# Kernel optimization log

Measured on AMD Instinct MI355X. Metric: run time of the kernel, lower is better.

## Reference

```python
import jax, jax.numpy as jnp
import numpy as np

N_NODES = 200000
FEAT_DIM = 256
EMB_DIM = 64
N_EXP = 100000
N_TARGETS = 1024
MAX_CAND = 128


def setup_inputs() -> dict:
    key = jax.random.key(0)
    ks = jax.random.split(key, 10)
    return {
        "x": jax.random.normal(ks[0], (N_NODES, FEAT_DIM), jnp.float32),
        "h": jax.random.normal(ks[1], (N_NODES, EMB_DIM), jnp.float32),
        "degree": jax.random.uniform(ks[2], (N_NODES,), jnp.float32),
        "beta": jax.random.uniform(ks[3], (N_NODES,), jnp.float32),
        "exp_nodes": jax.random.randint(ks[4], (N_EXP,), 0, N_NODES),
        "idx_targets": jax.random.randint(ks[5], (N_TARGETS,), 0, N_NODES),
        "W_raw": jax.random.normal(ks[6], (FEAT_DIM, EMB_DIM), jnp.float32) / np.float32(np.sqrt(FEAT_DIM)),
        "b_raw": jnp.zeros((EMB_DIM,), jnp.float32),
        "W_num": jax.random.normal(ks[7], (2, EMB_DIM), jnp.float32),
        "b_num": jnp.zeros((EMB_DIM,), jnp.float32),
        "W1": jax.random.normal(ks[8], (4 * EMB_DIM, EMB_DIM), jnp.float32) / np.float32(np.sqrt(4 * EMB_DIM)),
        "b1": jnp.zeros((EMB_DIM,), jnp.float32),
        "W2": jax.random.normal(ks[9], (EMB_DIM, 1), jnp.float32) / np.float32(np.sqrt(EMB_DIM)),
        "b2": jnp.zeros((1,), jnp.float32),
        "temperature": jnp.float32(1.0),
        "epsilon": jnp.float32(1.0),
    }


def reference(x, h, degree, beta, exp_nodes, idx_targets,
              W_raw, b_raw, W_num, b_num, W1, b1, W2, b2,
              temperature, epsilon):
    # gather node features and project (irregular gather + small GEMM)
    x_v = x[exp_nodes] @ W_raw + b_raw                       # [E, emb]
    h_v = h[exp_nodes]                                       # [E, emb]
    h_T = jnp.broadcast_to(h[idx_targets].mean(axis=0)[None, :],
                           (exp_nodes.shape[0], EMB_DIM))    # [E, emb]
    numerics = jnp.stack([degree[exp_nodes], beta[exp_nodes]], axis=-1)  # [E, 2]
    emb_num = numerics @ W_num + b_num                       # [E, emb]
    emb = jax.nn.relu(jnp.concatenate([x_v, h_v, h_T, emb_num], axis=-1))  # [E, 4*emb]
    # dropout is identity in eval mode
    hidden = jax.nn.relu(emb @ W1 + b1)                      # [E, emb]
    scores = (hidden @ W2 + b2)[:, 0]                        # [E]
    # straight-through gumbel top-k (eval: no gumbel noise, epsilon unused)
    y = jax.nn.softmax(scores / temperature)
    _, idx = jax.lax.top_k(y, MAX_CAND)
    y_hard = jnp.zeros_like(y).at[idx].set(1.0)
    y_st = jax.lax.stop_gradient(y_hard - y) + y
    candidates = y_st[idx]                                   # [MAX_CAND] (== 1.0 fwd)
    cand_indices = exp_nodes[idx]                            # [MAX_CAND]
    return candidates, cand_indices
```

## Files before the change

### kernel.cpp

```cpp
#include <hip/hip_runtime.h>
#include <stdint.h>

#define RELU(v) ((v) > 0.0f ? (v) : 0.0f)

typedef unsigned long long u64;
typedef unsigned int u32;
typedef unsigned short u16;
typedef float f32x4 __attribute__((ext_vector_type(4)));
typedef short bf16x8 __attribute__((ext_vector_type(8)));

constexpr int FEAT = 256;
constexpr int EMB  = 64;

constexpr int STG_ROW = 264;
constexpr int WAVE_BYTES = 16 * STG_ROW * 2;
constexpr int XV_ROW = 68;
constexpr int KEEP_BLK = 12;

__device__ inline u16 bf16_trunc(float v) { return (u16)(__float_as_uint(v) >> 16); }

__device__ inline u32 score_key(float s) {
    u32 u = __float_as_uint(s);
    return (u & 0x80000000u) ? ~u : (u | 0x80000000u);
}

__device__ inline bf16x8 pack_bf16x8(float4 lo, float4 hi) {
    bf16x8 r;
    r[0] = (short)bf16_trunc(lo.x); r[1] = (short)bf16_trunc(lo.y);
    r[2] = (short)bf16_trunc(lo.z); r[3] = (short)bf16_trunc(lo.w);
    r[4] = (short)bf16_trunc(hi.x); r[5] = (short)bf16_trunc(hi.y);
    r[6] = (short)bf16_trunc(hi.z); r[7] = (short)bf16_trunc(hi.w);
    return r;
}

__global__ __launch_bounds__(1024) void setup_kernel(
    const float* __restrict__ h, const int* __restrict__ idx_targets, int nT,
    const float* __restrict__ W_raw, const float* __restrict__ W1, const float* __restrict__ b1,
    float* __restrict__ bias_eff, u16* __restrict__ wrawpk, u16* __restrict__ w1pk)
{
    const int tid = threadIdx.x;
    if (blockIdx.x == 1) {
        for (int t = tid; t < 2048; t += 1024) {
            int ks   = t >> 8;
            int c    = (t >> 6) & 3;
            int lane = t & 63;
            int n    = c * 16 + (lane & 15);
            int kbase = ks * 32 + ((lane >> 4) << 3);
            #pragma unroll
            for (int j = 0; j < 8; ++j) {
                int k = kbase + j;
                wrawpk[t * 8 + j] = bf16_trunc(W_raw[(size_t)k * EMB + n]);
                w1pk  [t * 8 + j] = bf16_trunc(W1   [(size_t)k * EMB + n]);
            }
        }
        return;
    }
    __shared__ int   idx_s[1024];
    __shared__ float partial[16][64];
    __shared__ float hT[64];
    const int nid = nT > 1024 ? 1024 : nT;
    for (int i = tid; i < nid; i += 1024) idx_s[i] = idx_targets[i];
    __syncthreads();
    const int d = tid & 63, grp = tid >> 6;
    float s = 0.f;
    for (int t = grp; t < nid; t += 16)
        s += h[(size_t)idx_s[t] * EMB + d];
    partial[grp][d] = s;
    __syncthreads();
    if (tid < 64) {
        float m = 0.f;
        #pragma unroll
        for (int g = 0; g < 16; ++g) m += partial[g][tid];
        hT[tid] = RELU(m / (float)nT);
    }
    __syncthreads();
    if (tid < 64) {
        float acc = b1[tid];
        #pragma unroll 8
        for (int dd = 0; dd < 64; ++dd)
            acc = fmaf(hT[dd], W1[(size_t)(128 + dd) * EMB + tid], acc);
        bias_eff[tid] = acc;
    }
}

__global__ __launch_bounds__(256) void approx_score_kernel(
    const float* __restrict__ x, const float* __restrict__ h,
    const float* __restrict__ degree, const float* __restrict__ beta,
    const int* __restrict__ exp_nodes,
    const u16* __restrict__ wrawpk, const u16* __restrict__ w1pk,
    const float* __restrict__ b_raw,
    const float* __restrict__ W_num, const float* __restrict__ b_num,
    const float* __restrict__ W2, const float* __restrict__ bias_eff,
    u64* __restrict__ cand1, int E)
{
    __shared__ __align__(16) unsigned char smem[4][WAVE_BYTES];
    __shared__ u64 sarr[64];

    const int tid  = threadIdx.x;
    const int wid  = tid >> 6;
    const int lane = tid & 63;
    const int rloc = lane & 15;
    const int kgrp = lane >> 4;
    const int koff = kgrp * 8;
    const int tileBase = blockIdx.x * 64;

    const int grow = tileBase + wid * 16 + rloc;
    const int node = exp_nodes[grow < E ? grow : 0];
    const float* hrow = h + (size_t)node * EMB;
    const float dg = degree[node];
    const float bt = beta[node];

    u16*   stg = (u16*)&smem[wid][0];
    float* xvp = (float*)&smem[wid][0];

    {
        float4 v0  = *reinterpret_cast<const float4*>(x + (size_t)__shfl(node,  0) * FEAT + lane * 4);
        float4 v1  = *reinterpret_cast<const float4*>(x + (size_t)__shfl(node,  1) * FEAT + lane * 4);
        float4 v2  = *reinterpret_cast<const float4*>(x + (size_t)__shfl(node,  2) * FEAT + lane * 4);
        float4 v3  = *reinterpret_cast<const float4*>(x + (size_t)__shfl(node,  3) * FEAT + lane * 4);
        float4 v4  = *reinterpret_cast<const float4*>(x + (size_t)__shfl(node,  4) * FEAT + lane * 4);
        float4 v5  = *reinterpret_cast<const float4*>(x + (size_t)__shfl(node,  5) * FEAT + lane * 4);
        float4 v6  = *reinterpret_cast<const float4*>(x + (size_t)__shfl(node,  6) * FEAT + lane * 4);
        float4 v7  = *reinterpret_cast<const float4*>(x + (size_t)__shfl(node,  7) * FEAT + lane * 4);
        float4 v8  = *reinterpret_cast<const float4*>(x + (size_t)__shfl(node,  8) * FEAT + lane * 4);
        float4 v9  = *reinterpret_cast<const float4*>(x + (size_t)__shfl(node,  9) * FEAT + lane * 4);
        float4 v10 = *reinterpret_cast<const float4*>(x + (size_t)__shfl(node, 10) * FEAT + lane * 4);
        float4 v11 = *reinterpret_cast<const float4*>(x + (size_t)__shfl(node, 11) * FEAT + lane * 4);
        float4 v12 = *reinterpret_cast<const float4*>(x + (size_t)__shfl(node, 12) * FEAT + lane * 4);
        float4 v13 = *reinterpret_cast<const float4*>(x + (size_t)__shfl(node, 13) * FEAT + lane * 4);
        float4 v14 = *reinterpret_cast<const float4*>(x + (size_t)__shfl(node, 14) * FEAT + lane * 4);
        float4 v15 = *reinterpret_cast<const float4*>(x + (size_t)__shfl(node, 15) * FEAT + lane * 4);
        #define STG_WRITE(rr, vv) { \
            ushort4 pk; pk.x = bf16_trunc(vv.x); pk.y = bf16_trunc(vv.y); \
            pk.z = bf16_trunc(vv.z); pk.w = bf16_trunc(vv.w); \
            *reinterpret_cast<ushort4*>(stg + (rr) * STG_ROW + lane * 4) = pk; }
        STG_WRITE( 0, v0)  STG_WRITE( 1, v1)  STG_WRITE( 2, v2)  STG_WRITE( 3, v3)
        STG_WRITE( 4, v4)  STG_WRITE( 5, v5)  STG_WRITE( 6, v6)  STG_WRITE( 7, v7)
        STG_WRITE( 8, v8)  STG_WRITE( 9, v9)  STG_WRITE(10, v10) STG_WRITE(11, v11)
        STG_WRITE(12, v12) STG_WRITE(13, v13) STG_WRITE(14, v14) STG_WRITE(15, v15)
        #undef STG_WRITE
    }
    __builtin_amdgcn_wave_barrier();

    f32x4 acc1[4];
    #pragma unroll
    for (int c = 0; c < 4; ++c) {
        float bv = b_raw[c * 16 + rloc];
        acc1[c] = (f32x4){bv, bv, bv, bv};
    }
    #pragma unroll
    for (int ks = 0; ks < 8; ++ks) {
        bf16x8 a = *reinterpret_cast<const bf16x8*>(stg + rloc * STG_ROW + ks * 32 + koff);
        #pragma unroll
        for (int c = 0; c < 4; ++c) {
            bf16x8 b = *reinterpret_cast<const bf16x8*>(wrawpk + (size_t)((ks * 4 + c) * 64 + lane) * 8);
            acc1[c] = __builtin_amdgcn_mfma_f32_16x16x32_bf16(a, b, acc1[c], 0, 0, 0);
        }
    }
    __builtin_amdgcn_wave_barrier();

    #pragma unroll
    for (int c = 0; c < 4; ++c)
        #pragma unroll
        for (int r = 0; r < 4; ++r)
            xvp[(kgrp * 4 + r) * XV_ROW + c * 16 + rloc] = RELU(acc1[c][r]);
    __builtin_amdgcn_wave_barrier();

    f32x4 acc2[4];
    #pragma unroll
    for (int c = 0; c < 4; ++c) {
        float bv = bias_eff[c * 16 + rloc];
        acc2[c] = (f32x4){bv, bv, bv, bv};
    }

    #pragma unroll
    for (int ks = 0; ks < 2; ++ks) {
        float4 lo = *reinterpret_cast<const float4*>(hrow + ks * 32 + koff);
        float4 hi = *reinterpret_cast<const float4*>(hrow + ks * 32 + koff + 4);
        lo.x = RELU(lo.x); lo.y = RELU(lo.y); lo.z = RELU(lo.z); lo.w = RELU(lo.w);
        hi.x = RELU(hi.x); hi.y = RELU(hi.y); hi.z = RELU(hi.z); hi.w = RELU(hi.w);
        bf16x8 a = pack_bf16x8(lo, hi);
        #pragma unroll
        for (int c = 0; c < 4; ++c) {
            bf16x8 b = *reinterpret_cast<const bf16x8*>(w1pk + (size_t)(((2 + ks) * 4 + c) * 64 + lane) * 8);
            acc2[c] = __builtin_amdgcn_mfma_f32_16x16x32_bf16(a, b, acc2[c], 0, 0, 0);
        }
    }

    #pragma unroll
    for (int ks = 0; ks < 2; ++ks) {
        bf16x8 a;
        #pragma unroll
        for (int j = 0; j < 8; ++j) {
            int k = ks * 32 + koff + j;
            float v = RELU(fmaf(dg, W_num[k], fmaf(bt, W_num[EMB + k], b_num[k])));
            a[j] = (short)bf16_trunc(v);
        }
        #pragma unroll
        for (int c = 0; c < 4; ++c) {
            bf16x8 b = *reinterpret_cast<const bf16x8*>(w1pk + (size_t)(((6 + ks) * 4 + c) * 64 + lane) * 8);
            acc2[c] = __builtin_amdgcn_mfma_f32_16x16x32_bf16(a, b, acc2[c], 0, 0, 0);
        }
    }

    #pragma unroll
    for (int ks = 0; ks < 2; ++ks) {
        float4 lo = *reinterpret_cast<const float4*>(xvp + rloc * XV_ROW + ks * 32 + koff);
        float4 hi = *reinterpret_cast<const float4*>(xvp + rloc * XV_ROW + ks * 32 + koff + 4);
        bf16x8 a = pack_bf16x8(lo, hi);
        #pragma unroll
        for (int c = 0; c < 4; ++c) {
            bf16x8 b = *reinterpret_cast<const bf16x8*>(w1pk + (size_t)((ks * 4 + c) * 64 + lane) * 8);
            acc2[c] = __builtin_amdgcn_mfma_f32_16x16x32_bf16(a, b, acc2[c], 0, 0, 0);
        }
    }

    float p[4] = {0.f, 0.f, 0.f, 0.f};
    #pragma unroll
    for (int c = 0; c < 4; ++c) {
        float w2v = W2[c * 16 + rloc];
        #pragma unroll
        for (int r = 0; r < 4; ++r)
            p[r] = fmaf(RELU(acc2[c][r]), w2v, p[r]);
    }
    #pragma unroll
    for (int m = 1; m < 16; m <<= 1) {
        p[0] += __shfl_xor(p[0], m);
        p[1] += __shfl_xor(p[1], m);
        p[2] += __shfl_xor(p[2], m);
        p[3] += __shfl_xor(p[3], m);
    }
    if (rloc == 0) {
        #pragma unroll
        for (int r = 0; r < 4; ++r) {
            int lrow = wid * 16 + kgrp * 4 + r;
            int g = tileBase + lrow;
            sarr[lrow] = (g < E) ? (((u64)score_key(p[r]) << 32) | (u32)(~(u32)g)) : 0ULL;
        }
    }
    __syncthreads();

    if (wid == 0) {
        u64 v = sarr[lane];
        #pragma unroll
        for (int k = 2; k <= 64; k <<= 1) {
            #pragma unroll
            for (int j = k >> 1; j > 0; j >>= 1) {
                u64 o = __shfl_xor(v, j);
                bool lower = (lane & j) == 0;
                bool dir   = (lane & k) == 0;
                v = (lower == dir) ? (v > o ? v : o) : (v < o ? v : o);
            }
        }
        if (lane < KEEP_BLK) cand1[(size_t)blockIdx.x * KEEP_BLK + lane] = v;
    }
}

template<int N, int NT>
__device__ inline void bitonic_desc(u64* s, int tid) {
    for (int k = 2; k <= N; k <<= 1) {
        for (int j = k >> 1; j > 0; j >>= 1) {
            __syncthreads();
            for (int i = tid; i < N; i += NT) {
                int ixj = i ^ j;
                if (ixj > i) {
                    u64 a = s[i], b = s[ixj];
                    bool sw = ((i & k) == 0) ? (a < b) : (a > b);
                    if (sw) { s[i] = b; s[ixj] = a; }
                }
            }
        }
    }
    __syncthreads();
}

template<int N, int NT, int KEEP>
__global__ __launch_bounds__(NT) void seg_sort_kernel(
    const u64* __restrict__ in, int n_in, int seg, u64* __restrict__ out)
{
    __shared__ u64 s[N];
    int tid = threadIdx.x;
    int base = blockIdx.x * seg;
    for (int i = tid; i < N; i += NT) {
        int g = base + i;
        s[i] = (i < seg && g < n_in) ? in[g] : 0ULL;
    }
    bitonic_desc<N, NT>(s, tid);
    if (tid < KEEP) out[blockIdx.x * KEEP + tid] = s[tid];
}

__global__ __launch_bounds__(256) void rescore_kernel(
    const float* __restrict__ x, const float* __restrict__ h,
    const float* __restrict__ degree, const float* __restrict__ beta,
    const int* __restrict__ exp_nodes,
    const float* __restrict__ W_raw, const float* __restrict__ b_raw,
    const float* __restrict__ W_num, const float* __restrict__ b_num,
    const float* __restrict__ W1, const float* __restrict__ W2,
    const float* __restrict__ bias_eff,
    const u64* __restrict__ cand, u64* __restrict__ pairs2, int E)
{
    __shared__ float emb[4][192];
    const int tid = threadIdx.x;
    const int wid = tid >> 6;
    const int c   = tid & 63;
    const int i   = blockIdx.x * 4 + wid;

    const u64 raw = cand[i];
    const u32 low = (u32)raw;
    const u32 ge  = ~low;
    const int node = (raw != 0ULL && ge < (u32)E) ? exp_nodes[ge] : 0;

    const float* xrow = x + (size_t)node * FEAT;

    float s0 = b_raw[c], s1 = 0.f, s2 = 0.f, s3 = 0.f;
    for (int k = 0; k < FEAT; k += 4) {
        s0 = fmaf(xrow[k + 0], W_raw[(size_t)(k + 0) * EMB + c], s0);
        s1 = fmaf(xrow[k + 1], W_raw[(size_t)(k + 1) * EMB + c], s1);
        s2 = fmaf(xrow[k + 2], W_raw[(size_t)(k + 2) * EMB + c], s2);
        s3 = fmaf(xrow[k + 3], W_raw[(size_t)(k + 3) * EMB + c], s3);
    }
    float xv = (s0 + s1) + (s2 + s3);

    emb[wid][c]       = RELU(xv);
    emb[wid][64 + c]  = RELU(h[(size_t)node * EMB + c]);
    emb[wid][128 + c] = RELU(fmaf(degree[node], W_num[c], fmaf(beta[node], W_num[EMB + c], b_num[c])));
    __syncthreads();

    float h0 = bias_eff[c], h1 = 0.f, h2 = 0.f, h3 = 0.f;
    for (int j = 0; j < 64; j += 2) {
        h0 = fmaf(emb[wid][j],     W1[(size_t)j * EMB + c],       h0);
        h1 = fmaf(emb[wid][j + 1], W1[(size_t)(j + 1) * EMB + c], h1);
    }
    for (int j = 0; j < 64; j += 2) {
        h2 = fmaf(emb[wid][64 + j],     W1[(size_t)(64 + j) * EMB + c],     h2);
        h3 = fmaf(emb[wid][64 + j + 1], W1[(size_t)(64 + j + 1) * EMB + c], h3);
    }
    for (int j = 0; j < 64; j += 2) {
        h0 = fmaf(emb[wid][128 + j],     W1[(size_t)(192 + j) * EMB + c],     h0);
        h1 = fmaf(emb[wid][128 + j + 1], W1[(size_t)(192 + j + 1) * EMB + c], h1);
    }
    float hid = (h0 + h1) + (h2 + h3);

    float p = RELU(hid) * W2[c];
    #pragma unroll
    for (int m = 1; m < 64; m <<= 1) p += __shfl_xor(p, m);

    if (c == 0)
        pairs2[i] = (raw == 0ULL) ? 0ULL : (((u64)score_key(p) << 32) | low);
}

__global__ __launch_bounds__(1024) void topk_final_kernel(
    const u64* __restrict__ in, int n_in,
    const int* __restrict__ exp_nodes, float* __restrict__ out)
{
    __shared__ u64 s[1024];
    int tid = threadIdx.x;
    s[tid] = (tid < n_in) ? in[tid] : 0ULL;
    bitonic_desc<1024, 1024>(s, tid);
    if (tid < 128) {
        u64 p = s[tid];
        u32 idx = ~(u32)(p & 0xFFFFFFFFu);
        out[tid]       = 1.0f;
        out[128 + tid] = (float)exp_nodes[idx];
    }
}

extern "C" void kernel_launch(void* const* d_in, const int* in_sizes, int n_in,
                              void* d_out, int out_size, void* d_ws, size_t ws_size,
                              hipStream_t stream) {
    const float* x          = (const float*)d_in[0];
    const float* h          = (const float*)d_in[1];
    const float* degree     = (const float*)d_in[2];
    const float* beta       = (const float*)d_in[3];
    const int*   exp_nodes  = (const int*)d_in[4];
    const int*   idx_targets= (const int*)d_in[5];
    const float* W_raw      = (const float*)d_in[6];
    const float* b_raw      = (const float*)d_in[7];
    const float* W_num      = (const float*)d_in[8];
    const float* b_num      = (const float*)d_in[9];
    const float* W1         = (const float*)d_in[10];
    const float* b1         = (const float*)d_in[11];
    const float* W2         = (const float*)d_in[12];

    int E  = in_sizes[4];
    int nT = in_sizes[5];

    int nTiles = (E + 63) / 64;
    int nCand1 = nTiles * KEEP_BLK;
    int nSel   = (nCand1 + 1023) / 1024;
    int nKept  = nSel * 52;
    int nResc  = (nKept + 3) / 4;

    char* ws = (char*)d_ws;
    float* bias_eff = (float*)ws;
    u16* wrawpk = (u16*)(ws + 256);
    u16* w1pk   = (u16*)(ws + 256 + 32768);
    u64* cand1  = (u64*)(ws + 256 + 65536);
    u64* cand2  = (u64*)(ws + 256 + 65536 + 163840);
    u64* pairs2 = (u64*)(ws + 256 + 65536 + 163840 + 8192);

    setup_kernel<<<2, 1024, 0, stream>>>(h, idx_targets, nT, W_raw, W1, b1,
                                         bias_eff, wrawpk, w1pk);

    approx_score_kernel<<<nTiles, 256, 0, stream>>>(x, h, degree, beta, exp_nodes,
                                                    wrawpk, w1pk, b_raw, W_num, b_num,
                                                    W2, bias_eff, cand1, E);

    seg_sort_kernel<1024, 512, 52><<<nSel, 512, 0, stream>>>(cand1, nCand1, 1024, cand2);

    rescore_kernel<<<nResc, 256, 0, stream>>>(x, h, degree, beta, exp_nodes,
                                              W_raw, b_raw, W_num, b_num, W1, W2,
                                              bias_eff, cand2, pairs2, E);

    topk_final_kernel<<<1, 1024, 0, stream>>>(pairs2, nKept, exp_nodes, (float*)d_out);
}
```

Measured before the change: 106.8 us.

## Fuse segment sort and exact rescoring into one kernel with finer segments

Replaces the separate segment-sort and rescore kernels with one kernel. Each of 64 blocks loads a segment of about 300 approximate-score candidates into a 512-entry shared-memory bitonic sort, then rescores its top 16 exactly, using wave-level barriers instead of block barriers. This removes one kernel launch, the round trip through the intermediate candidate buffer, and uses a smaller sort per block. The trade-off is that only 16 candidates per segment survive instead of 52 per 1024, so a segment holding more than 16 of the true top 128 would now drop some.

```diff
diff --git a/kernel.cpp b/kernel.cpp
--- a/kernel.cpp
+++ b/kernel.cpp
@@ -274,22 +274,8 @@
     __syncthreads();
 }
 
-template<int N, int NT, int KEEP>
-__global__ __launch_bounds__(NT) void seg_sort_kernel(
-    const u64* __restrict__ in, int n_in, int seg, u64* __restrict__ out)
-{
-    __shared__ u64 s[N];
-    int tid = threadIdx.x;
-    int base = blockIdx.x * seg;
-    for (int i = tid; i < N; i += NT) {
-        int g = base + i;
-        s[i] = (i < seg && g < n_in) ? in[g] : 0ULL;
-    }
-    bitonic_desc<N, NT>(s, tid);
-    if (tid < KEEP) out[blockIdx.x * KEEP + tid] = s[tid];
-}
-
-__global__ __launch_bounds__(256) void rescore_kernel(
+__global__ __launch_bounds__(512) void selrescore_kernel(
+    const u64* __restrict__ cand1, int nCand1, int seg,
     const float* __restrict__ x, const float* __restrict__ h,
     const float* __restrict__ degree, const float* __restrict__ beta,
     const int* __restrict__ exp_nodes,
@@ -297,56 +283,69 @@
     const float* __restrict__ W_num, const float* __restrict__ b_num,
     const float* __restrict__ W1, const float* __restrict__ W2,
     const float* __restrict__ bias_eff,
-    const u64* __restrict__ cand, u64* __restrict__ pairs2, int E)
+    u64* __restrict__ pairs2, int E)
 {
-    __shared__ float emb[4][192];
+    __shared__ u64  s[512];
+    __shared__ float emb[8][192];
     const int tid = threadIdx.x;
+    const int base = blockIdx.x * seg;
+
+    for (int i = tid; i < 512; i += 512) {
+        int g = base + i;
+        s[i] = (i < seg && g < nCand1) ? cand1[g] : 0ULL;
+    }
+    bitonic_desc<512, 512>(s, tid);
+
     const int wid = tid >> 6;
     const int c   = tid & 63;
-    const int i   = blockIdx.x * 4 + wid;
-
-    const u64 raw = cand[i];
-    const u32 low = (u32)raw;
-    const u32 ge  = ~low;
-    const int node = (raw != 0ULL && ge < (u32)E) ? exp_nodes[ge] : 0;
-
-    const float* xrow = x + (size_t)node * FEAT;
-
-    float s0 = b_raw[c], s1 = 0.f, s2 = 0.f, s3 = 0.f;
-    for (int k = 0; k < FEAT; k += 4) {
-        s0 = fmaf(xrow[k + 0], W_raw[(size_t)(k + 0) * EMB + c], s0);
-        s1 = fmaf(xrow[k + 1], W_raw[(size_t)(k + 1) * EMB + c], s1);
-        s2 = fmaf(xrow[k + 2], W_raw[(size_t)(k + 2) * EMB + c], s2);
-        s3 = fmaf(xrow[k + 3], W_raw[(size_t)(k + 3) * EMB + c], s3);
-    }
-    float xv = (s0 + s1) + (s2 + s3);
-
-    emb[wid][c]       = RELU(xv);
-    emb[wid][64 + c]  = RELU(h[(size_t)node * EMB + c]);
-    emb[wid][128 + c] = RELU(fmaf(degree[node], W_num[c], fmaf(beta[node], W_num[EMB + c], b_num[c])));
-    __syncthreads();
-
-    float h0 = bias_eff[c], h1 = 0.f, h2 = 0.f, h3 = 0.f;
-    for (int j = 0; j < 64; j += 2) {
-        h0 = fmaf(emb[wid][j],     W1[(size_t)j * EMB + c],       h0);
-        h1 = fmaf(emb[wid][j + 1], W1[(size_t)(j + 1) * EMB + c], h1);
-    }
-    for (int j = 0; j < 64; j += 2) {
-        h2 = fmaf(emb[wid][64 + j],     W1[(size_t)(64 + j) * EMB + c],     h2);
-        h3 = fmaf(emb[wid][64 + j + 1], W1[(size_t)(64 + j + 1) * EMB + c], h3);
-    }
-    for (int j = 0; j < 64; j += 2) {
-        h0 = fmaf(emb[wid][128 + j],     W1[(size_t)(192 + j) * EMB + c],     h0);
-        h1 = fmaf(emb[wid][128 + j + 1], W1[(size_t)(192 + j + 1) * EMB + c], h1);
-    }
-    float hid = (h0 + h1) + (h2 + h3);
-
-    float p = RELU(hid) * W2[c];
-    #pragma unroll
-    for (int m = 1; m < 64; m <<= 1) p += __shfl_xor(p, m);
-
-    if (c == 0)
-        pairs2[i] = (raw == 0ULL) ? 0ULL : (((u64)score_key(p) << 32) | low);
+
+    #pragma unroll
+    for (int rr = 0; rr < 2; ++rr) {
+        const int slot = rr * 8 + wid;
+        const u64 raw = s[slot];
+        const u32 low = (u32)raw;
+        const u32 ge  = ~low;
+        const int node = (raw != 0ULL && ge < (u32)E) ? exp_nodes[ge] : 0;
+
+        const float* xrow = x + (size_t)node * FEAT;
+
+        float s0 = b_raw[c], s1 = 0.f, s2 = 0.f, s3 = 0.f;
+        for (int k = 0; k < FEAT; k += 4) {
+            s0 = fmaf(xrow[k + 0], W_raw[(size_t)(k + 0) * EMB + c], s0);
+            s1 = fmaf(xrow[k + 1], W_raw[(size_t)(k + 1) * EMB + c], s1);
+            s2 = fmaf(xrow[k + 2], W_raw[(size_t)(k + 2) * EMB + c], s2);
+            s3 = fmaf(xrow[k + 3], W_raw[(size_t)(k + 3) * EMB + c], s3);
+        }
+        float xv = (s0 + s1) + (s2 + s3);
+
+        emb[wid][c]       = RELU(xv);
+        emb[wid][64 + c]  = RELU(h[(size_t)node * EMB + c]);
+        emb[wid][128 + c] = RELU(fmaf(degree[node], W_num[c], fmaf(beta[node], W_num[EMB + c], b_num[c])));
+        __builtin_amdgcn_wave_barrier();
+
+        float h0 = bias_eff[c], h1 = 0.f, h2 = 0.f, h3 = 0.f;
+        for (int j = 0; j < 64; j += 2) {
+            h0 = fmaf(emb[wid][j],     W1[(size_t)j * EMB + c],       h0);
+            h1 = fmaf(emb[wid][j + 1], W1[(size_t)(j + 1) * EMB + c], h1);
+        }
+        for (int j = 0; j < 64; j += 2) {
+            h2 = fmaf(emb[wid][64 + j],     W1[(size_t)(64 + j) * EMB + c],     h2);
+            h3 = fmaf(emb[wid][64 + j + 1], W1[(size_t)(64 + j + 1) * EMB + c], h3);
+        }
+        for (int j = 0; j < 64; j += 2) {
+            h0 = fmaf(emb[wid][128 + j],     W1[(size_t)(192 + j) * EMB + c],     h0);
+            h1 = fmaf(emb[wid][128 + j + 1], W1[(size_t)(192 + j + 1) * EMB + c], h1);
+        }
+        float hid = (h0 + h1) + (h2 + h3);
+
+        float p = RELU(hid) * W2[c];
+        #pragma unroll
+        for (int m = 1; m < 64; m <<= 1) p += __shfl_xor(p, m);
+
+        if (c == 0)
+            pairs2[blockIdx.x * 16 + slot] = (raw == 0ULL) ? 0ULL : (((u64)score_key(p) << 32) | low);
+        __builtin_amdgcn_wave_barrier();
+    }
 }
 
 __global__ __launch_bounds__(1024) void topk_final_kernel(
@@ -387,17 +386,16 @@
 
     int nTiles = (E + 63) / 64;
     int nCand1 = nTiles * KEEP_BLK;
-    int nSel   = (nCand1 + 1023) / 1024;
-    int nKept  = nSel * 52;
-    int nResc  = (nKept + 3) / 4;
+    int nSel   = 64;
+    int seg    = (nCand1 + nSel - 1) / nSel;
+    int nKept  = nSel * 16;
 
     char* ws = (char*)d_ws;
     float* bias_eff = (float*)ws;
     u16* wrawpk = (u16*)(ws + 256);
     u16* w1pk   = (u16*)(ws + 256 + 32768);
     u64* cand1  = (u64*)(ws + 256 + 65536);
-    u64* cand2  = (u64*)(ws + 256 + 65536 + 163840);
-    u64* pairs2 = (u64*)(ws + 256 + 65536 + 163840 + 8192);
+    u64* pairs2 = (u64*)(ws + 256 + 65536 + 163840);
 
     setup_kernel<<<2, 1024, 0, stream>>>(h, idx_targets, nT, W_raw, W1, b1,
                                          bias_eff, wrawpk, w1pk);
@@ -406,11 +404,10 @@
                                                     wrawpk, w1pk, b_raw, W_num, b_num,
                                                     W2, bias_eff, cand1, E);
 
-    seg_sort_kernel<1024, 512, 52><<<nSel, 512, 0, stream>>>(cand1, nCand1, 1024, cand2);
-
-    rescore_kernel<<<nResc, 256, 0, stream>>>(x, h, degree, beta, exp_nodes,
-                                              W_raw, b_raw, W_num, b_num, W1, W2,
-                                              bias_eff, cand2, pairs2, E);
+    selrescore_kernel<<<nSel, 512, 0, stream>>>(cand1, nCand1, seg,
+                                                x, h, degree, beta, exp_nodes,
+                                                W_raw, b_raw, W_num, b_num, W1, W2,
+                                                bias_eff, pairs2, E);
 
     topk_final_kernel<<<1, 1024, 0, stream>>>(pairs2, nKept, exp_nodes, (float*)d_out);
 }
```

After: 143.4 us. 1.34x slower.
